# Kernel optimization log

Measured on AMD Instinct MI355X. Metric: run time of the kernel, lower is better.

The kernel has to match this reference:

```python
import jax, jax.numpy as jnp
import numpy as np

N_NODES = 50000


def _gcn_layer(x, edge_index, W, b, relu):
    """tf_geometric-style GCN: h = D^-1/2 (A+I) D^-1/2 (x @ W) + b, opt relu."""
    n = x.shape[0]
    h = x @ W  # [N, D_out] transform first (standard GCN)
    src, dst = edge_index[0], edge_index[1]
    sl = jnp.arange(n, dtype=src.dtype)
    src = jnp.concatenate([src, sl])  # add self-loops (renorm trick)
    dst = jnp.concatenate([dst, sl])
    deg = jax.ops.segment_sum(jnp.ones_like(dst, dtype=h.dtype), dst, num_segments=n)
    dinv = jax.lax.rsqrt(jnp.maximum(deg, 1e-12))
    norm = dinv[src] * dinv[dst]  # symmetric normalization per edge
    msg = h[src] * norm[:, None]  # [E+N, D_out] gather + scale
    out = jax.ops.segment_sum(msg, dst, num_segments=n) + b
    return jax.nn.relu(out) if relu else out


def setup_inputs() -> dict:
    key = jax.random.key(0)
    ks = jax.random.split(key, 12)
    F, E = 512, 800000
    d = {}
    d["x"] = jax.random.normal(ks[0], (N_NODES, F), dtype=jnp.float32)
    d["edge_index1"] = jax.random.randint(ks[1], (2, E), 0, N_NODES, dtype=jnp.int32)
    d["edge_index2"] = jax.random.randint(ks[2], (2, E), 0, N_NODES, dtype=jnp.int32)
    def glorot(k, shape):
        lim = np.sqrt(6.0 / (shape[0] + shape[1])).astype(np.float32)
        return jax.random.uniform(k, shape, jnp.float32, -lim, lim)
    d["W10"] = glorot(ks[3], (F, 256)); d["b10"] = jnp.zeros((256,), jnp.float32)
    d["W20"] = glorot(ks[4], (F, 64));  d["b20"] = jnp.zeros((64,), jnp.float32)
    d["W21"] = glorot(ks[5], (64, 256)); d["b21"] = jnp.zeros((256,), jnp.float32)
    d["Wfc"] = glorot(ks[6], (256, 16)); d["bfc"] = jnp.zeros((16,), jnp.float32)
    return d


def reference(x, edge_index1, edge_index2, W10, b10, W20, b20, W21, b21, Wfc, bfc):
    h1 = _gcn_layer(x, edge_index1, W10, b10, relu=True)   # GCN(256, relu)
    h2 = _gcn_layer(x, edge_index2, W20, b20, relu=False)  # GCN(64)
    h2 = _gcn_layer(h2, edge_index2, W21, b21, relu=True)  # GCN(256, relu)
    h = h1 + h2
    return h @ Wfc + bfc  # Dense(class_num)
```

## Files before the change

kernel.cpp:

```cpp
#include <hip/hip_runtime.h>
#include <hip/hip_bf16.h>
#include <cstdint>
#include <cstddef>

#define N_NODES 50000
#define FDIM 512
#define NBKT 391
#define CHUNK 8192
#define BCAP 4096

typedef __bf16 bf16_t;
typedef bf16_t bf16x8 __attribute__((ext_vector_type(8)));
typedef float f32x4 __attribute__((ext_vector_type(4)));

__device__ __forceinline__ unsigned short f2bf(float f) {
  union { float f; uint32_t u; } c; c.f = f;
  uint32_t u = c.u;
  uint32_t r = (u + 0x7fffu + ((u >> 16) & 1u)) >> 16;
  return (unsigned short)r;
}
__device__ __forceinline__ float bf2f(unsigned short u) {
  union { uint32_t i; float f; } c; c.i = (uint32_t)u << 16; return c.f;
}
__device__ __forceinline__ float4 ld_bf4(const unsigned short* p) {
  ushort4 u = *(const ushort4*)p;
  float4 r; r.x = bf2f(u.x); r.y = bf2f(u.y); r.z = bf2f(u.z); r.w = bf2f(u.w);
  return r;
}
__device__ __forceinline__ void async16(const void* g, void* l) {
  __builtin_amdgcn_global_load_lds((const __attribute__((address_space(1))) void*)g,
                                   (__attribute__((address_space(3))) void*)l, 16, 0, 0);
}

__global__ __launch_bounds__(256) void binA(const int* __restrict__ d1, const int* __restrict__ d2,
                                            int* __restrict__ M1, int* __restrict__ M2,
                                            int E1, int E2, int nch1, int nch2) {
  const int g = blockIdx.y;
  const int* dst = g ? d2 : d1;
  int* M = g ? M2 : M1;
  const int E = g ? E2 : E1;
  const int nch = g ? nch2 : nch1;
  const int chunk = blockIdx.x;
  if (chunk >= nch) return;
  __shared__ int cnt[NBKT];
  for (int j = threadIdx.x; j < NBKT; j += 256) cnt[j] = 0;
  __syncthreads();
  const int base = chunk * CHUNK;
#pragma unroll 4
  for (int i = 0; i < CHUNK / 256; i++) {
    int e = base + i * 256 + threadIdx.x;
    if (e < E) atomicAdd(&cnt[dst[e] >> 7], 1);
  }
  __syncthreads();
  for (int j = threadIdx.x; j < NBKT; j += 256) M[chunk * NBKT + j] = cnt[j];
}

__global__ __launch_bounds__(512) void bin_offsets(int* __restrict__ M1, int* __restrict__ M2,
                                                   int* __restrict__ bases,
                                                   int nch1, int nch2, int E1, int E2) {
  const int g = blockIdx.x;
  int* M = g ? M2 : M1;
  const int nch = g ? nch2 : nch1;
  int* base = bases + g * (NBKT + 1);
  const int E = g ? E2 : E1;
  const int t = threadIdx.x;
  __shared__ int tot[512];
  int running = 0;
  if (t < NBKT) {
    for (int b = 0; b < nch; b++) {
      int v = M[b * NBKT + t];
      M[b * NBKT + t] = running;
      running += v;
    }
  }
  tot[t] = (t < NBKT) ? running : 0;
  __syncthreads();
  for (int off = 1; off < 512; off <<= 1) {
    int u = (t >= off) ? tot[t - off] : 0;
    __syncthreads();
    tot[t] += u;
    __syncthreads();
  }
  int ex = (t == 0) ? 0 : tot[t - 1];
  if (t < NBKT) {
    base[t] = ex;
    for (int b = 0; b < nch; b++) M[b * NBKT + t] += ex;
  }
  if (t == NBKT) base[NBKT] = E;
}

__global__ __launch_bounds__(256) void binB(const int* __restrict__ s1, const int* __restrict__ d1,
                                            const int* __restrict__ M1, unsigned* __restrict__ eb1,
                                            int E1, int nch1,
                                            const int* __restrict__ s2, const int* __restrict__ d2,
                                            const int* __restrict__ M2, unsigned* __restrict__ eb2,
                                            int E2, int nch2) {
  const int g = blockIdx.y;
  const int* src = g ? s2 : s1;
  const int* dst = g ? d2 : d1;
  const int* M = g ? M2 : M1;
  unsigned* eb = g ? eb2 : eb1;
  const int E = g ? E2 : E1;
  const int nch = g ? nch2 : nch1;
  const int chunk = blockIdx.x;
  if (chunk >= nch) return;
  __shared__ int gbase[NBKT];
  __shared__ int cur[NBKT];
  for (int j = threadIdx.x; j < NBKT; j += 256) {
    gbase[j] = M[chunk * NBKT + j];
    cur[j] = 0;
  }
  __syncthreads();
  const int base = chunk * CHUNK;
#pragma unroll 4
  for (int i = 0; i < CHUNK / 256; i++) {
    int e = base + i * 256 + threadIdx.x;
    if (e < E) {
      int d = dst[e];
      int b = d >> 7;
      int pos = gbase[b] + atomicAdd(&cur[b], 1);
      eb[pos] = ((unsigned)d << 16) | (unsigned)src[e];
    }
  }
}

__global__ __launch_bounds__(256) void binC(const unsigned* __restrict__ eb1,
                                            const unsigned* __restrict__ eb2,
                                            const int* __restrict__ bases,
                                            int* __restrict__ rp1, float* __restrict__ dv1,
                                            int* __restrict__ cs1,
                                            int* __restrict__ rp2, float* __restrict__ dv2,
                                            int* __restrict__ cs2, int n) {
  const int g = blockIdx.y;
  const unsigned* eb = g ? eb2 : eb1;
  const int* base = bases + g * (NBKT + 1);
  int* rp = g ? rp2 : rp1;
  float* dv = g ? dv2 : dv1;
  int* cs = g ? cs2 : cs1;
  const int bkt = blockIdx.x;
  const int e0 = base[bkt], e1 = base[bkt + 1];
  const int cnt = e1 - e0;
  const int node0 = bkt << 7;
  const int t = threadIdx.x;
  __shared__ unsigned stage[BCAP];
  __shared__ int sorted[BCAP];
  __shared__ int dcnt[128], dcur[128], dscan[128];
  if (t < 128) dcnt[t] = 0;
  __syncthreads();
  for (int i = t; i < cnt; i += 256) {
    unsigned pe = eb[e0 + i];
    stage[i] = pe;
    atomicAdd(&dcnt[(pe >> 16) & 127], 1);
  }
  __syncthreads();
  if (t < 128) dscan[t] = dcnt[t];
  __syncthreads();
  for (int off = 1; off < 128; off <<= 1) {
    int u = (t < 128 && t >= off) ? dscan[t - off] : 0;
    __syncthreads();
    if (t < 128) dscan[t] += u;
    __syncthreads();
  }
  if (t < 128) {
    int ex = dscan[t] - dcnt[t];
    dcur[t] = ex;
    int node = node0 + t;
    if (node < n) {
      rp[node] = e0 + ex;
      dv[node] = rsqrtf((float)dcnt[t] + 1.0f);
    }
  }
  __syncthreads();
  for (int i = t; i < cnt; i += 256) {
    unsigned pe = stage[i];
    int d = (pe >> 16) & 127;
    int pos = atomicAdd(&dcur[d], 1);
    sorted[pos] = (int)(pe & 0xFFFFu);
  }
  __syncthreads();
  for (int i = t; i < cnt; i += 256) cs[e0 + i] = sorted[i];
  if (bkt == NBKT - 1 && t == 0) rp[n] = base[NBKT];
}

__global__ void cvt_x(const float4* __restrict__ X, ushort4* __restrict__ out, int n4) {
  int stride = gridDim.x * 256;
  for (int i = blockIdx.x * 256 + threadIdx.x; i < n4; i += stride) {
    float4 v = X[i];
    ushort4 o;
    o.x = f2bf(v.x); o.y = f2bf(v.y); o.z = f2bf(v.z); o.w = f2bf(v.w);
    out[i] = o;
  }
}

__global__ void cvt_w(const float* __restrict__ W10, const float* __restrict__ W20,
                      const float* __restrict__ W21, unsigned short* __restrict__ WcatT,
                      unsigned short* __restrict__ W21T) {
  int j = blockIdx.x * 256 + threadIdx.x;
  const int T1 = 384 * 512;
  if (j < T1) {
    int n = j >> 9, k = j & 511;
    float v = (n < 256) ? W10[k * 256 + n] : ((n < 320) ? W20[k * 64 + (n - 256)] : 0.f);
    WcatT[j] = f2bf(v);
  } else {
    int j2 = j - T1;
    if (j2 < 256 * 64) {
      int n = j2 >> 6, k = j2 & 63;
      W21T[j2] = f2bf(W21[k * 256 + n]);
    }
  }
}

template <int KTOT, int SPLIT>
__global__ __launch_bounds__(256) void gemm_bt(const unsigned short* __restrict__ A,
                                               const unsigned short* __restrict__ B,
                                               void* __restrict__ o1, void* __restrict__ o2,
                                               int M, int NLIM) {
  __shared__ unsigned short As[128 * 64];
  __shared__ unsigned short Bs[128 * 64];
  const int tid = threadIdx.x;
  const int w = tid >> 6, lane = tid & 63;
  const int row0 = blockIdx.x * 128;
  const int n0 = blockIdx.y * 128;
  const int wm = w >> 1, wn = w & 1;
  const int lr = lane >> 3, lc8 = (lane & 7) * 8;
  const int mlane = lane & 15, q = lane >> 4;

  f32x4 acc[4][4];
#pragma unroll
  for (int mi = 0; mi < 4; mi++)
#pragma unroll
    for (int ni = 0; ni < 4; ni++) {
      f32x4 z = {0.f, 0.f, 0.f, 0.f};
      acc[mi][ni] = z;
    }

  for (int k0 = 0; k0 < KTOT; k0 += 64) {
    __syncthreads();
#pragma unroll
    for (int i = 0; i < 4; i++) {
      int gr = row0 + i * 32 + w * 8 + lr;
      if (gr > M - 1) gr = M - 1;
      async16(A + (size_t)gr * KTOT + k0 + lc8, &As[(i * 32 + w * 8) * 64]);
    }
#pragma unroll
    for (int i = 0; i < 4; i++) {
      int n = i * 32 + w * 8 + lr;
      async16(B + (size_t)(n0 + n) * KTOT + k0 + lc8, &Bs[(i * 32 + w * 8) * 64]);
    }
    __syncthreads();
#pragma unroll
    for (int kk = 0; kk < 2; kk++) {
      bf16x8 af[4], bfr[4];
#pragma unroll
      for (int mi = 0; mi < 4; mi++)
        af[mi] = *(const bf16x8*)&As[(wm * 64 + mi * 16 + mlane) * 64 + kk * 32 + q * 8];
#pragma unroll
      for (int ni = 0; ni < 4; ni++)
        bfr[ni] = *(const bf16x8*)&Bs[(wn * 64 + ni * 16 + mlane) * 64 + kk * 32 + q * 8];
#pragma unroll
      for (int mi = 0; mi < 4; mi++)
#pragma unroll
        for (int ni = 0; ni < 4; ni++)
          acc[mi][ni] = __builtin_amdgcn_mfma_f32_16x16x32_bf16(af[mi], bfr[ni], acc[mi][ni], 0, 0, 0);
    }
  }

#pragma unroll
  for (int mi = 0; mi < 4; mi++)
#pragma unroll
    for (int ni = 0; ni < 4; ni++) {
      int c = n0 + wn * 64 + ni * 16 + mlane;
#pragma unroll
      for (int rg = 0; rg < 4; rg++) {
        int r = row0 + wm * 64 + mi * 16 + q * 4 + rg;
        if (r < M) {
          float v = acc[mi][ni][rg];
          if (SPLIT) {
            if (c < 256) ((unsigned short*)o1)[(size_t)r * 256 + c] = f2bf(v);
            else if (c < NLIM) ((unsigned short*)o2)[(size_t)r * 64 + (c - 256)] = f2bf(v);
          } else {
            ((float*)o1)[(size_t)r * 256 + c] = v;
          }
        }
      }
    }
}

__global__ __launch_bounds__(256) void prop256(const unsigned short* __restrict__ H,
                                               const int* __restrict__ rp,
                                               const int* __restrict__ cs,
                                               const float* __restrict__ dinv,
                                               const float* __restrict__ bias,
                                               float* __restrict__ out, int n) {
  const int i = blockIdx.x * 4 + (threadIdx.x >> 6);
  const int l = threadIdx.x & 63;
  if (i >= n) return;
  const float di = dinv[i];
  float4 self = ld_bf4(H + (size_t)i * 256 + l * 4);
  float4 acc;
  acc.x = di * self.x; acc.y = di * self.y; acc.z = di * self.z; acc.w = di * self.w;
  const int e1 = rp[i + 1];
#pragma unroll 4
  for (int e = rp[i]; e < e1; e++) {
    int s = cs[e];
    float wgt = dinv[s];
    float4 rrow = ld_bf4(H + (size_t)s * 256 + l * 4);
    acc.x += wgt * rrow.x; acc.y += wgt * rrow.y; acc.z += wgt * rrow.z; acc.w += wgt * rrow.w;
  }
  float4 b = *(const float4*)(bias + l * 4);
  float4 o;
  o.x = fmaxf(di * acc.x + b.x, 0.f);
  o.y = fmaxf(di * acc.y + b.y, 0.f);
  o.z = fmaxf(di * acc.z + b.z, 0.f);
  o.w = fmaxf(di * acc.w + b.w, 0.f);
  *(float4*)(out + (size_t)i * 256 + l * 4) = o;
}

template <int BIAS>
__global__ __launch_bounds__(256) void prop64(const unsigned short* __restrict__ H,
                                              const int* __restrict__ rp,
                                              const int* __restrict__ cs,
                                              const float* __restrict__ dinv,
                                              const float* __restrict__ bias,
                                              unsigned short* __restrict__ out, int n) {
  const int i = blockIdx.x * 16 + (threadIdx.x >> 4);
  const int l = threadIdx.x & 15;
  if (i >= n) return;
  const float di = dinv[i];
  float4 self = ld_bf4(H + (size_t)i * 64 + l * 4);
  float4 acc;
  acc.x = di * self.x; acc.y = di * self.y; acc.z = di * self.z; acc.w = di * self.w;
  const int e1 = rp[i + 1];
#pragma unroll 4
  for (int e = rp[i]; e < e1; e++) {
    int s = cs[e];
    float wgt = dinv[s];
    float4 rrow = ld_bf4(H + (size_t)s * 64 + l * 4);
    acc.x += wgt * rrow.x; acc.y += wgt * rrow.y; acc.z += wgt * rrow.z; acc.w += wgt * rrow.w;
  }
  float4 o;
  o.x = di * acc.x; o.y = di * acc.y; o.z = di * acc.z; o.w = di * acc.w;
  if (BIAS) {
    float4 b = *(const float4*)(bias + l * 4);
    o.x += b.x; o.y += b.y; o.z += b.z; o.w += b.w;
  }
  ushort4 ob;
  ob.x = f2bf(o.x); ob.y = f2bf(o.y); ob.z = f2bf(o.z); ob.w = f2bf(o.w);
  *(ushort4*)(out + (size_t)i * 64 + l * 4) = ob;
}

__global__ __launch_bounds__(256) void final_k(const float* __restrict__ h1,
                                               const float* __restrict__ h3,
                                               const float* __restrict__ b21,
                                               const float* __restrict__ Wfc,
                                               const float* __restrict__ bfc,
                                               float* __restrict__ out, int M) {
  __shared__ float hs[16][260];
  __shared__ float wt[16][260];
  __shared__ float bs[16];
  const int t = threadIdx.x;
  for (int j = t; j < 4096; j += 256) { int k = j >> 4, c = j & 15; wt[c][k] = Wfc[j]; }
  if (t < 16) bs[t] = bfc[t];
  const float bb = b21[t];
  const int node0 = blockIdx.x * 16;
#pragma unroll
  for (int nl = 0; nl < 16; nl++) {
    int i = node0 + nl;
    float v = 0.f;
    if (i < M) {
      size_t o = (size_t)i * 256 + t;
      v = fmaxf(h3[o] + bb, 0.f) + h1[o];
    }
    hs[nl][t] = v;
  }
  __syncthreads();
  const int nl = t >> 4, c = t & 15;
  const int i = node0 + nl;
  if (i >= M) return;
  const float4* hp = (const float4*)&hs[nl][0];
  const float4* wp = (const float4*)&wt[c][0];
  float s = bs[c];
#pragma unroll 8
  for (int k4 = 0; k4 < 64; k4++) {
    float4 a = hp[k4], b = wp[k4];
    s += a.x * b.x + a.y * b.y + a.z * b.z + a.w * b.w;
  }
  out[(size_t)i * 16 + c] = s;
}

extern "C" void kernel_launch(void* const* d_in, const int* in_sizes, int n_in,
                              void* d_out, int out_size, void* d_ws, size_t ws_size,
                              hipStream_t stream) {
  const float* X   = (const float*)d_in[0];
  const int*   ei1 = (const int*)d_in[1];
  const int*   ei2 = (const int*)d_in[2];
  const float* W10 = (const float*)d_in[3];
  const float* b10 = (const float*)d_in[4];
  const float* W20 = (const float*)d_in[5];
  const float* b20 = (const float*)d_in[6];
  const float* W21 = (const float*)d_in[7];
  const float* b21 = (const float*)d_in[8];
  const float* Wfc = (const float*)d_in[9];
  const float* bfc = (const float*)d_in[10];
  float* out = (float*)d_out;

  const int N = N_NODES;
  const int E1 = in_sizes[1] / 2, E2 = in_sizes[2] / 2;
  const int* src1 = ei1; const int* dst1 = ei1 + E1;
  const int* src2 = ei2; const int* dst2 = ei2 + E2;
  const int nch1 = (E1 + CHUNK - 1) / CHUNK, nch2 = (E2 + CHUNK - 1) / CHUNK;
  const int nchmax = (nch1 > nch2) ? nch1 : nch2;

  char* p = (char*)d_ws;
  auto alloc = [&](size_t b) { char* r = p; p += (b + 255) & ~(size_t)255; return (void*)r; };
  int* M1 = (int*)alloc((size_t)nch1 * NBKT * 4);
  int* M2 = (int*)alloc((size_t)nch2 * NBKT * 4);
  int* bases = (int*)alloc((size_t)2 * (NBKT + 1) * 4);
  unsigned* eb1 = (unsigned*)alloc((size_t)E1 * 4);
  unsigned* eb2 = (unsigned*)alloc((size_t)E2 * 4);
  int* rp1 = (int*)alloc((size_t)(N + 1) * 4);
  int* rp2 = (int*)alloc((size_t)(N + 1) * 4);
  float* dinv1 = (float*)alloc((size_t)N * 4);
  float* dinv2 = (float*)alloc((size_t)N * 4);
  int* csr1s = (int*)alloc((size_t)E1 * 4);
  int* csr2s = (int*)alloc((size_t)E2 * 4);
  unsigned short* WcatT = (unsigned short*)alloc(384 * 512 * 2);
  unsigned short* W21T  = (unsigned short*)alloc(256 * 64 * 2);
  unsigned short* Xb = (unsigned short*)alloc((size_t)N * 512 * 2);
  float* h1 = (float*)Xb;
  unsigned short* Xh1b = (unsigned short*)alloc((size_t)N * 256 * 2);
  unsigned short* Xh2b = (unsigned short*)alloc((size_t)N * 64 * 2);
  unsigned short* h2b  = (unsigned short*)alloc((size_t)N * 64 * 2);
  unsigned short* q2b  = (unsigned short*)alloc((size_t)N * 64 * 2);
  float* h3 = (float*)alloc((size_t)N * 256 * 4);

  binA<<<dim3(nchmax, 2), 256, 0, stream>>>(dst1, dst2, M1, M2, E1, E2, nch1, nch2);
  bin_offsets<<<dim3(2), 512, 0, stream>>>(M1, M2, bases, nch1, nch2, E1, E2);
  binB<<<dim3(nchmax, 2), 256, 0, stream>>>(src1, dst1, M1, eb1, E1, nch1,
                                            src2, dst2, M2, eb2, E2, nch2);
  binC<<<dim3(NBKT, 2), 256, 0, stream>>>(eb1, eb2, bases, rp1, dinv1, csr1s,
                                          rp2, dinv2, csr2s, N);
  cvt_x<<<dim3(4096), 256, 0, stream>>>((const float4*)X, (ushort4*)Xb, N * FDIM / 4);
  cvt_w<<<dim3((384 * 512 + 256 * 64 + 255) / 256), 256, 0, stream>>>(W10, W20, W21, WcatT, W21T);
  gemm_bt<512, 1><<<dim3((N + 127) / 128, 3), 256, 0, stream>>>(Xb, WcatT, Xh1b, Xh2b, N, 320);
  prop256<<<dim3((N + 3) / 4), 256, 0, stream>>>(Xh1b, rp1, csr1s, dinv1, b10, h1, N);
  prop64<1><<<dim3((N + 15) / 16), 256, 0, stream>>>(Xh2b, rp2, csr2s, dinv2, b20, h2b, N);
  prop64<0><<<dim3((N + 15) / 16), 256, 0, stream>>>(h2b, rp2, csr2s, dinv2, nullptr, q2b, N);
  gemm_bt<64, 0><<<dim3((N + 127) / 128, 2), 256, 0, stream>>>(q2b, W21T, h3, nullptr, N, 256);
  final_k<<<dim3((N + 15) / 16), 256, 0, stream>>>(h1, h3, b21, Wfc, bfc, out, N);
}
```

Measured before the change: 473.1 us.

## Fuse X conversion into GEMM, prescale by dinv, fuse second GEMM with final dense

The separate fp32-to-bf16 conversion of X is removed and folded into the first GEMM, which now loads fp32 X directly and uses a wider 192-column tile so two column blocks cover the 384 padded outputs. The GEMM epilogue multiplies each row by the source dinv, which lets the propagation kernels drop the per-edge dinv gather and the multiply. h1 is now stored in bf16 instead of fp32. The W21 GEMM, bias, ReLU, the h1 addition and the final 16-wide dense layer are merged into one MFMA kernel, so the fp32 h3 intermediate no longer round-trips through memory. Together these cut memory traffic and kernel count, at the cost of extra bf16 rounding of h1 and of the final hidden state.

```diff
diff --git a/kernel.cpp b/kernel.cpp
--- a/kernel.cpp
+++ b/kernel.cpp
@@ -182,85 +182,87 @@
   if (bkt == NBKT - 1 && t == 0) rp[n] = base[NBKT];
 }
 
-__global__ void cvt_x(const float4* __restrict__ X, ushort4* __restrict__ out, int n4) {
-  int stride = gridDim.x * 256;
-  for (int i = blockIdx.x * 256 + threadIdx.x; i < n4; i += stride) {
-    float4 v = X[i];
-    ushort4 o;
-    o.x = f2bf(v.x); o.y = f2bf(v.y); o.z = f2bf(v.z); o.w = f2bf(v.w);
-    out[i] = o;
-  }
-}
-
 __global__ void cvt_w(const float* __restrict__ W10, const float* __restrict__ W20,
-                      const float* __restrict__ W21, unsigned short* __restrict__ WcatT,
-                      unsigned short* __restrict__ W21T) {
+                      const float* __restrict__ W21, const float* __restrict__ Wfc,
+                      unsigned short* __restrict__ WcatT, unsigned short* __restrict__ W21T,
+                      unsigned short* __restrict__ WfcT) {
   int j = blockIdx.x * 256 + threadIdx.x;
-  const int T1 = 384 * 512;
+  const int T1 = 384 * 512, T2 = 256 * 64, T3 = 16 * 256;
   if (j < T1) {
     int n = j >> 9, k = j & 511;
     float v = (n < 256) ? W10[k * 256 + n] : ((n < 320) ? W20[k * 64 + (n - 256)] : 0.f);
     WcatT[j] = f2bf(v);
-  } else {
+  } else if (j < T1 + T2) {
     int j2 = j - T1;
-    if (j2 < 256 * 64) {
-      int n = j2 >> 6, k = j2 & 63;
-      W21T[j2] = f2bf(W21[k * 256 + n]);
-    }
-  }
-}
-
-template <int KTOT, int SPLIT>
-__global__ __launch_bounds__(256) void gemm_bt(const unsigned short* __restrict__ A,
-                                               const unsigned short* __restrict__ B,
-                                               void* __restrict__ o1, void* __restrict__ o2,
-                                               int M, int NLIM) {
+    int n = j2 >> 6, k = j2 & 63;
+    W21T[j2] = f2bf(W21[k * 256 + n]);
+  } else if (j < T1 + T2 + T3) {
+    int j3 = j - T1 - T2;
+    int c = j3 >> 8, k = j3 & 255;
+    WfcT[j3] = f2bf(Wfc[k * 16 + c]);
+  }
+}
+
+__global__ __launch_bounds__(256) void gemm_x(const float* __restrict__ X,
+                                              const unsigned short* __restrict__ WcatT,
+                                              const float* __restrict__ dinv1,
+                                              const float* __restrict__ dinv2,
+                                              unsigned short* __restrict__ Xh1b,
+                                              unsigned short* __restrict__ Xh2b, int M) {
   __shared__ unsigned short As[128 * 64];
-  __shared__ unsigned short Bs[128 * 64];
+  __shared__ unsigned short Bs[192 * 64];
   const int tid = threadIdx.x;
   const int w = tid >> 6, lane = tid & 63;
   const int row0 = blockIdx.x * 128;
-  const int n0 = blockIdx.y * 128;
+  const int n0 = blockIdx.y * 192;
   const int wm = w >> 1, wn = w & 1;
   const int lr = lane >> 3, lc8 = (lane & 7) * 8;
   const int mlane = lane & 15, q = lane >> 4;
 
-  f32x4 acc[4][4];
+  f32x4 acc[4][6];
 #pragma unroll
   for (int mi = 0; mi < 4; mi++)
 #pragma unroll
-    for (int ni = 0; ni < 4; ni++) {
+    for (int ni = 0; ni < 6; ni++) {
       f32x4 z = {0.f, 0.f, 0.f, 0.f};
       acc[mi][ni] = z;
     }
 
-  for (int k0 = 0; k0 < KTOT; k0 += 64) {
-    __syncthreads();
-#pragma unroll
-    for (int i = 0; i < 4; i++) {
-      int gr = row0 + i * 32 + w * 8 + lr;
-      if (gr > M - 1) gr = M - 1;
-      async16(A + (size_t)gr * KTOT + k0 + lc8, &As[(i * 32 + w * 8) * 64]);
-    }
-#pragma unroll
-    for (int i = 0; i < 4; i++) {
-      int n = i * 32 + w * 8 + lr;
-      async16(B + (size_t)(n0 + n) * KTOT + k0 + lc8, &Bs[(i * 32 + w * 8) * 64]);
+  for (int k0 = 0; k0 < 512; k0 += 64) {
+    __syncthreads();
+#pragma unroll
+    for (int j = 0; j < 4; j++) {
+      int idx = j * 512 + tid;
+      (void)idx;
+    }
+#pragma unroll
+    for (int j = 0; j < 8; j++) {
+      int idx = j * 256 + tid;
+      int r = idx >> 4, f4 = idx & 15;
+      int gr = row0 + r; if (gr > M - 1) gr = M - 1;
+      float4 v = *(const float4*)(X + (size_t)gr * 512 + k0 + f4 * 4);
+      ushort4 o; o.x = f2bf(v.x); o.y = f2bf(v.y); o.z = f2bf(v.z); o.w = f2bf(v.w);
+      *(ushort4*)&As[r * 64 + f4 * 4] = o;
+    }
+#pragma unroll
+    for (int j = 0; j < 6; j++) {
+      int r = j * 32 + w * 8 + lr;
+      async16(WcatT + (size_t)(n0 + r) * 512 + k0 + lc8, &Bs[(j * 32 + w * 8) * 64]);
     }
     __syncthreads();
 #pragma unroll
     for (int kk = 0; kk < 2; kk++) {
-      bf16x8 af[4], bfr[4];
+      bf16x8 af[4], bfr[6];
 #pragma unroll
       for (int mi = 0; mi < 4; mi++)
         af[mi] = *(const bf16x8*)&As[(wm * 64 + mi * 16 + mlane) * 64 + kk * 32 + q * 8];
 #pragma unroll
-      for (int ni = 0; ni < 4; ni++)
-        bfr[ni] = *(const bf16x8*)&Bs[(wn * 64 + ni * 16 + mlane) * 64 + kk * 32 + q * 8];
+      for (int ni = 0; ni < 6; ni++)
+        bfr[ni] = *(const bf16x8*)&Bs[(wn * 96 + ni * 16 + mlane) * 64 + kk * 32 + q * 8];
 #pragma unroll
       for (int mi = 0; mi < 4; mi++)
 #pragma unroll
-        for (int ni = 0; ni < 4; ni++)
+        for (int ni = 0; ni < 6; ni++)
           acc[mi][ni] = __builtin_amdgcn_mfma_f32_16x16x32_bf16(af[mi], bfr[ni], acc[mi][ni], 0, 0, 0);
     }
   }
@@ -268,20 +270,16 @@
 #pragma unroll
   for (int mi = 0; mi < 4; mi++)
 #pragma unroll
-    for (int ni = 0; ni < 4; ni++) {
-      int c = n0 + wn * 64 + ni * 16 + mlane;
-#pragma unroll
-      for (int rg = 0; rg < 4; rg++) {
-        int r = row0 + wm * 64 + mi * 16 + q * 4 + rg;
-        if (r < M) {
-          float v = acc[mi][ni][rg];
-          if (SPLIT) {
-            if (c < 256) ((unsigned short*)o1)[(size_t)r * 256 + c] = f2bf(v);
-            else if (c < NLIM) ((unsigned short*)o2)[(size_t)r * 64 + (c - 256)] = f2bf(v);
-          } else {
-            ((float*)o1)[(size_t)r * 256 + c] = v;
-          }
-        }
+    for (int rg = 0; rg < 4; rg++) {
+      int r = row0 + wm * 64 + mi * 16 + q * 4 + rg;
+      if (r >= M) continue;
+      float dv1 = dinv1[r], dv2 = dinv2[r];
+#pragma unroll
+      for (int ni = 0; ni < 6; ni++) {
+        int c = n0 + wn * 96 + ni * 16 + mlane;
+        float v = acc[mi][ni][rg];
+        if (c < 256) Xh1b[(size_t)r * 256 + c] = f2bf(v * dv1);
+        else if (c < 320) Xh2b[(size_t)r * 64 + (c - 256)] = f2bf(v * dv2);
       }
     }
 }
@@ -291,32 +289,28 @@
                                                const int* __restrict__ cs,
                                                const float* __restrict__ dinv,
                                                const float* __restrict__ bias,
-                                               float* __restrict__ out, int n) {
+                                               unsigned short* __restrict__ out, int n) {
   const int i = blockIdx.x * 4 + (threadIdx.x >> 6);
   const int l = threadIdx.x & 63;
   if (i >= n) return;
   const float di = dinv[i];
-  float4 self = ld_bf4(H + (size_t)i * 256 + l * 4);
-  float4 acc;
-  acc.x = di * self.x; acc.y = di * self.y; acc.z = di * self.z; acc.w = di * self.w;
+  float4 acc = ld_bf4(H + (size_t)i * 256 + l * 4);
   const int e1 = rp[i + 1];
-#pragma unroll 4
+#pragma unroll 8
   for (int e = rp[i]; e < e1; e++) {
-    int s = cs[e];
-    float wgt = dinv[s];
-    float4 rrow = ld_bf4(H + (size_t)s * 256 + l * 4);
-    acc.x += wgt * rrow.x; acc.y += wgt * rrow.y; acc.z += wgt * rrow.z; acc.w += wgt * rrow.w;
+    float4 rrow = ld_bf4(H + (size_t)cs[e] * 256 + l * 4);
+    acc.x += rrow.x; acc.y += rrow.y; acc.z += rrow.z; acc.w += rrow.w;
   }
   float4 b = *(const float4*)(bias + l * 4);
-  float4 o;
-  o.x = fmaxf(di * acc.x + b.x, 0.f);
-  o.y = fmaxf(di * acc.y + b.y, 0.f);
-  o.z = fmaxf(di * acc.z + b.z, 0.f);
-  o.w = fmaxf(di * acc.w + b.w, 0.f);
-  *(float4*)(out + (size_t)i * 256 + l * 4) = o;
-}
-
-template <int BIAS>
+  ushort4 o;
+  o.x = f2bf(fmaxf(di * acc.x + b.x, 0.f));
+  o.y = f2bf(fmaxf(di * acc.y + b.y, 0.f));
+  o.z = f2bf(fmaxf(di * acc.z + b.z, 0.f));
+  o.w = f2bf(fmaxf(di * acc.w + b.w, 0.f));
+  *(ushort4*)(out + (size_t)i * 256 + l * 4) = o;
+}
+
+template <int MODE>
 __global__ __launch_bounds__(256) void prop64(const unsigned short* __restrict__ H,
                                               const int* __restrict__ rp,
                                               const int* __restrict__ cs,
@@ -327,65 +321,117 @@
   const int l = threadIdx.x & 15;
   if (i >= n) return;
   const float di = dinv[i];
-  float4 self = ld_bf4(H + (size_t)i * 64 + l * 4);
-  float4 acc;
-  acc.x = di * self.x; acc.y = di * self.y; acc.z = di * self.z; acc.w = di * self.w;
+  float4 acc = ld_bf4(H + (size_t)i * 64 + l * 4);
   const int e1 = rp[i + 1];
-#pragma unroll 4
+#pragma unroll 8
   for (int e = rp[i]; e < e1; e++) {
-    int s = cs[e];
-    float wgt = dinv[s];
-    float4 rrow = ld_bf4(H + (size_t)s * 64 + l * 4);
-    acc.x += wgt * rrow.x; acc.y += wgt * rrow.y; acc.z += wgt * rrow.z; acc.w += wgt * rrow.w;
+    float4 rrow = ld_bf4(H + (size_t)cs[e] * 64 + l * 4);
+    acc.x += rrow.x; acc.y += rrow.y; acc.z += rrow.z; acc.w += rrow.w;
   }
   float4 o;
-  o.x = di * acc.x; o.y = di * acc.y; o.z = di * acc.z; o.w = di * acc.w;
-  if (BIAS) {
+  if (MODE) {
     float4 b = *(const float4*)(bias + l * 4);
-    o.x += b.x; o.y += b.y; o.z += b.z; o.w += b.w;
+    o.x = (di * acc.x + b.x) * di; o.y = (di * acc.y + b.y) * di;
+    o.z = (di * acc.z + b.z) * di; o.w = (di * acc.w + b.w) * di;
+  } else {
+    o.x = di * acc.x; o.y = di * acc.y; o.z = di * acc.z; o.w = di * acc.w;
   }
   ushort4 ob;
   ob.x = f2bf(o.x); ob.y = f2bf(o.y); ob.z = f2bf(o.z); ob.w = f2bf(o.w);
   *(ushort4*)(out + (size_t)i * 64 + l * 4) = ob;
 }
 
-__global__ __launch_bounds__(256) void final_k(const float* __restrict__ h1,
-                                               const float* __restrict__ h3,
-                                               const float* __restrict__ b21,
-                                               const float* __restrict__ Wfc,
-                                               const float* __restrict__ bfc,
-                                               float* __restrict__ out, int M) {
-  __shared__ float hs[16][260];
-  __shared__ float wt[16][260];
-  __shared__ float bs[16];
-  const int t = threadIdx.x;
-  for (int j = t; j < 4096; j += 256) { int k = j >> 4, c = j & 15; wt[c][k] = Wfc[j]; }
-  if (t < 16) bs[t] = bfc[t];
-  const float bb = b21[t];
-  const int node0 = blockIdx.x * 16;
-#pragma unroll
-  for (int nl = 0; nl < 16; nl++) {
-    int i = node0 + nl;
-    float v = 0.f;
-    if (i < M) {
-      size_t o = (size_t)i * 256 + t;
-      v = fmaxf(h3[o] + bb, 0.f) + h1[o];
-    }
-    hs[nl][t] = v;
-  }
-  __syncthreads();
-  const int nl = t >> 4, c = t & 15;
-  const int i = node0 + nl;
-  if (i >= M) return;
-  const float4* hp = (const float4*)&hs[nl][0];
-  const float4* wp = (const float4*)&wt[c][0];
-  float s = bs[c];
-#pragma unroll 8
-  for (int k4 = 0; k4 < 64; k4++) {
-    float4 a = hp[k4], b = wp[k4];
-    s += a.x * b.x + a.y * b.y + a.z * b.z + a.w * b.w;
-  }
-  out[(size_t)i * 16 + c] = s;
+__global__ __launch_bounds__(256) void gemm2_final(const unsigned short* __restrict__ q2,
+                                                   const unsigned short* __restrict__ W21T,
+                                                   const unsigned short* __restrict__ WfcT,
+                                                   const unsigned short* __restrict__ h1,
+                                                   const float* __restrict__ b21,
+                                                   const float* __restrict__ bfc,
+                                                   float* __restrict__ out, int M) {
+  __shared__ unsigned short As[64 * 64];
+  __shared__ unsigned short Bs[256 * 64];
+  __shared__ unsigned short Hs[64 * 256];
+  __shared__ unsigned short Ws[16 * 256];
+  const int tid = threadIdx.x;
+  const int w = tid >> 6, lane = tid & 63;
+  const int row0 = blockIdx.x * 64;
+  const int wm = w >> 1, wn = w & 1;
+  const int lr = lane >> 3, lc8 = (lane & 7) * 8;
+  const int mlane = lane & 15, q = lane >> 4;
+
+#pragma unroll
+  for (int j = 0; j < 2; j++) {
+    int r = j * 32 + w * 8 + lr;
+    int gr = row0 + r; if (gr > M - 1) gr = M - 1;
+    async16(q2 + (size_t)gr * 64 + lc8, &As[(j * 32 + w * 8) * 64]);
+  }
+#pragma unroll
+  for (int j = 0; j < 8; j++) {
+    int r = j * 32 + w * 8 + lr;
+    async16(W21T + (size_t)r * 64 + lc8, &Bs[(j * 32 + w * 8) * 64]);
+  }
+#pragma unroll
+  for (int j = 0; j < 2; j++) {
+    int base = (j * 4 + w) * 512;
+    async16(WfcT + base + lane * 8, &Ws[base]);
+  }
+  __syncthreads();
+
+  f32x4 acc[2][8];
+#pragma unroll
+  for (int mi = 0; mi < 2; mi++)
+#pragma unroll
+    for (int ni = 0; ni < 8; ni++) {
+      f32x4 z = {0.f, 0.f, 0.f, 0.f};
+      acc[mi][ni] = z;
+    }
+#pragma unroll
+  for (int kk = 0; kk < 2; kk++) {
+    bf16x8 af[2], bfr[8];
+#pragma unroll
+    for (int mi = 0; mi < 2; mi++)
+      af[mi] = *(const bf16x8*)&As[(wm * 32 + mi * 16 + mlane) * 64 + kk * 32 + q * 8];
+#pragma unroll
+    for (int ni = 0; ni < 8; ni++)
+      bfr[ni] = *(const bf16x8*)&Bs[(wn * 128 + ni * 16 + mlane) * 64 + kk * 32 + q * 8];
+#pragma unroll
+    for (int mi = 0; mi < 2; mi++)
+#pragma unroll
+      for (int ni = 0; ni < 8; ni++)
+        acc[mi][ni] = __builtin_amdgcn_mfma_f32_16x16x32_bf16(af[mi], bfr[ni], acc[mi][ni], 0, 0, 0);
+  }
+
+#pragma unroll
+  for (int mi = 0; mi < 2; mi++)
+#pragma unroll
+    for (int ni = 0; ni < 8; ni++) {
+      int c = wn * 128 + ni * 16 + mlane;
+      float bb = b21[c];
+#pragma unroll
+      for (int rg = 0; rg < 4; rg++) {
+        int rl = wm * 32 + mi * 16 + q * 4 + rg;
+        int gr = row0 + rl;
+        float v = 0.f;
+        if (gr < M)
+          v = fmaxf(acc[mi][ni][rg] + bb, 0.f) + bf2f(h1[(size_t)gr * 256 + c]);
+        Hs[rl * 256 + c] = f2bf(v);
+      }
+    }
+  __syncthreads();
+
+  f32x4 a2 = {0.f, 0.f, 0.f, 0.f};
+#pragma unroll
+  for (int k0 = 0; k0 < 8; k0++) {
+    bf16x8 af = *(const bf16x8*)&Hs[(w * 16 + mlane) * 256 + k0 * 32 + q * 8];
+    bf16x8 bfr = *(const bf16x8*)&Ws[mlane * 256 + k0 * 32 + q * 8];
+    a2 = __builtin_amdgcn_mfma_f32_16x16x32_bf16(af, bfr, a2, 0, 0, 0);
+  }
+  const float bo = bfc[mlane];
+#pragma unroll
+  for (int rg = 0; rg < 4; rg++) {
+    int gr = row0 + w * 16 + q * 4 + rg;
+    if (gr < M) out[(size_t)gr * 16 + mlane] = a2[rg] + bo;
+  }
 }
 
 extern "C" void kernel_launch(void* const* d_in, const int* in_sizes, int n_in,
@@ -426,13 +472,12 @@
   int* csr2s = (int*)alloc((size_t)E2 * 4);
   unsigned short* WcatT = (unsigned short*)alloc(384 * 512 * 2);
   unsigned short* W21T  = (unsigned short*)alloc(256 * 64 * 2);
-  unsigned short* Xb = (unsigned short*)alloc((size_t)N * 512 * 2);
-  float* h1 = (float*)Xb;
+  unsigned short* WfcT  = (unsigned short*)alloc(16 * 256 * 2);
   unsigned short* Xh1b = (unsigned short*)alloc((size_t)N * 256 * 2);
   unsigned short* Xh2b = (unsigned short*)alloc((size_t)N * 64 * 2);
   unsigned short* h2b  = (unsigned short*)alloc((size_t)N * 64 * 2);
   unsigned short* q2b  = (unsigned short*)alloc((size_t)N * 64 * 2);
-  float* h3 = (float*)alloc((size_t)N * 256 * 4);
+  unsigned short* h1b  = (unsigned short*)alloc((size_t)N * 256 * 2);
 
   binA<<<dim3(nchmax, 2), 256, 0, stream>>>(dst1, dst2, M1, M2, E1, E2, nch1, nch2);
   bin_offsets<<<dim3(2), 512, 0, stream>>>(M1, M2, bases, nch1, nch2, E1, E2);
@@ -440,12 +485,11 @@
                                             src2, dst2, M2, eb2, E2, nch2);
   binC<<<dim3(NBKT, 2), 256, 0, stream>>>(eb1, eb2, bases, rp1, dinv1, csr1s,
                                           rp2, dinv2, csr2s, N);
-  cvt_x<<<dim3(4096), 256, 0, stream>>>((const float4*)X, (ushort4*)Xb, N * FDIM / 4);
-  cvt_w<<<dim3((384 * 512 + 256 * 64 + 255) / 256), 256, 0, stream>>>(W10, W20, W21, WcatT, W21T);
-  gemm_bt<512, 1><<<dim3((N + 127) / 128, 3), 256, 0, stream>>>(Xb, WcatT, Xh1b, Xh2b, N, 320);
-  prop256<<<dim3((N + 3) / 4), 256, 0, stream>>>(Xh1b, rp1, csr1s, dinv1, b10, h1, N);
+  cvt_w<<<dim3((384 * 512 + 256 * 64 + 16 * 256 + 255) / 256), 256, 0, stream>>>(
+      W10, W20, W21, Wfc, WcatT, W21T, WfcT);
+  gemm_x<<<dim3((N + 127) / 128, 2), 256, 0, stream>>>(X, WcatT, dinv1, dinv2, Xh1b, Xh2b, N);
+  prop256<<<dim3((N + 3) / 4), 256, 0, stream>>>(Xh1b, rp1, csr1s, dinv1, b10, h1b, N);
   prop64<1><<<dim3((N + 15) / 16), 256, 0, stream>>>(Xh2b, rp2, csr2s, dinv2, b20, h2b, N);
   prop64<0><<<dim3((N + 15) / 16), 256, 0, stream>>>(h2b, rp2, csr2s, dinv2, nullptr, q2b, N);
-  gemm_bt<64, 0><<<dim3((N + 127) / 128, 2), 256, 0, stream>>>(q2b, W21T, h3, nullptr, N, 256);
-  final_k<<<dim3((N + 15) / 16), 256, 0, stream>>>(h1, h3, b21, Wfc, bfc, out, N);
-}
+  gemm2_final<<<dim3((N + 63) / 64), 256, 0, stream>>>(q2b, W21T, WfcT, h1b, b21, bfc, out, N);
+}
```

Result: no change. 476.6 us (+0.8%).
